# Kernel optimization log

Measured on AMD Instinct MI355X. Metric: run time of the kernel, lower is better.

## Reference

```python
import jax, jax.numpy as jnp
import numpy as np

N0, N1, N2 = 20000, 15000, 15000
N = N0 + N1 + N2          # total nodes
E = 800000                # edges
H, D = 4, 64              # heads, hidden per head
ED = 64                   # edge feature dim
NET = 8                   # num edge types
C = 16                    # num classes
SLOPE = 0.2               # leaky relu negative slope
ALPHA = 0.05              # residual-attention mixing

def _glorot(key, shape):
    return jax.random.normal(key, shape, dtype=jnp.float32) / jnp.sqrt(jnp.float32(shape[-1]))

def setup_inputs() -> dict:
    key = jax.random.key(0)
    ks = jax.random.split(key, 32)
    return {
        "x0": jax.random.normal(ks[0], (N0, 128), jnp.float32),
        "x1": jax.random.normal(ks[1], (N1, 64), jnp.float32),
        "x2": jax.random.normal(ks[2], (N2, 32), jnp.float32),
        "src": jax.random.randint(ks[3], (E,), 0, N),
        "dst": jax.random.randint(ks[4], (E,), 0, N),
        "efeat": jax.random.randint(ks[5], (E,), 0, NET),
        # per-node-type input projections (fc_list)
        "W0": _glorot(ks[6], (64, 128)), "b0": jnp.zeros((64,), jnp.float32),
        "W1": _glorot(ks[7], (64, 64)),  "b1": jnp.zeros((64,), jnp.float32),
        "W2": _glorot(ks[8], (64, 32)),  "b2": jnp.zeros((64,), jnp.float32),
        # GAT layer 0: in 64 -> H*D, no residual, elu
        "Wg0": _glorot(ks[9], (H * D, 64)),
        "etab0": _glorot(ks[10], (NET, ED)),
        "We0": _glorot(ks[11], (H * ED, ED)),
        "al0": _glorot(ks[12], (H, D)), "ar0": _glorot(ks[13], (H, D)), "ae0": _glorot(ks[14], (H, ED)),
        # GAT layer 1: in H*D -> H*D, identity residual, elu
        "Wg1": _glorot(ks[15], (H * D, H * D)),
        "etab1": _glorot(ks[16], (NET, ED)),
        "We1": _glorot(ks[17], (H * ED, ED)),
        "al1": _glorot(ks[18], (H, D)), "ar1": _glorot(ks[19], (H, D)), "ae1": _glorot(ks[20], (H, ED)),
        # final GAT layer: in H*D -> 1*C, linear residual, no activation
        "Wg2": _glorot(ks[21], (C, H * D)),
        "etab2": _glorot(ks[22], (NET, ED)),
        "We2": _glorot(ks[23], (ED, ED)),
        "al2": _glorot(ks[24], (1, C)), "ar2": _glorot(ks[25], (1, C)), "ae2": _glorot(ks[26], (1, ED)),
        "resW2": _glorot(ks[27], (C, H * D)),
    }

def _edge_softmax(scores, dst):
    # softmax over incoming edges of each dst node; scores: [E, H]
    m = jax.ops.segment_max(scores, dst, num_segments=N)
    ex = jnp.exp(scores - m[dst])
    s = jax.ops.segment_sum(ex, dst, num_segments=N)
    return ex / (s[dst] + 1e-9)

def _gat_conv(h, src, dst, et, Wg, etab, We, al, ar, ae, res_attn, res, resW, act):
    nH, oD = al.shape
    feat = (h @ Wg.T).reshape(N, nH, oD)                 # [N,H,D]
    ee = (etab[et] @ We.T).reshape(E, nH, -1)            # [E,H,ED]
    el = jnp.einsum('nhd,hd->nh', feat, al)
    er = jnp.einsum('nhd,hd->nh', feat, ar)
    es = jnp.einsum('ehd,hd->eh', ee, ae)
    logits = jax.nn.leaky_relu(el[src] + er[dst] + es, SLOPE)
    a = _edge_softmax(logits, dst)                       # [E,H]
    if res_attn is not None:
        a = a * (1.0 - ALPHA) + res_attn * ALPHA
    out = jax.ops.segment_sum(a[:, :, None] * feat[src], dst, num_segments=N)
    if res:
        resval = (h @ resW.T).reshape(N, -1, oD) if resW is not None else h.reshape(N, nH, oD)
        out = out + resval
    if act is not None:
        out = act(out)
    return out, jax.lax.stop_gradient(a)                 # attention detached (res_attn)

def reference(x0, x1, x2, src, dst, efeat, W0, b0, W1, b1, W2, b2,
              Wg0, etab0, We0, al0, ar0, ae0,
              Wg1, etab1, We1, al1, ar1, ae1,
              Wg2, etab2, We2, al2, ar2, ae2, resW2):
    h = jnp.concatenate([x0 @ W0.T + b0, x1 @ W1.T + b1, x2 @ W2.T + b2], axis=0)  # [N,64]
    h, ra = _gat_conv(h, src, dst, efeat, Wg0, etab0, We0, al0, ar0, ae0, None, False, None, jax.nn.elu)
    h = h.reshape(N, -1)
    h, ra = _gat_conv(h, src, dst, efeat, Wg1, etab1, We1, al1, ar1, ae1, ra, True, None, jax.nn.elu)
    h = h.reshape(N, -1)
    logits, _ = _gat_conv(h, src, dst, efeat, Wg2, etab2, We2, al2, ar2, ae2, None, True, resW2, None)
    return logits.mean(axis=1)                           # [N, C]
```

## Files before the change

kernel.cpp:

```cpp
#include <hip/hip_runtime.h>
#include <math.h>

#define N0 20000
#define N1 15000
#define N2 15000
#define NN 50000
#define EE 800000
#define SLOPE 0.2f
#define ALPHA 0.05f

typedef _Float16 h8 __attribute__((ext_vector_type(8)));
typedef _Float16 h4 __attribute__((ext_vector_type(4)));
typedef float f4v __attribute__((ext_vector_type(4)));

__device__ __forceinline__ float sel4(float4 v, int h) {
    float lo = (h & 1) ? v.y : v.x;
    float hi = (h & 1) ? v.w : v.z;
    return (h & 2) ? hi : lo;
}

__device__ __forceinline__ float elu_fast(float x) {
    return x > 0.f ? x : __expf(x) - 1.f;
}


__global__ void hist_kernel(const int* __restrict__ dst, int* __restrict__ deg, int E_) {
    int e = blockIdx.x * blockDim.x + threadIdx.x;
    if (e < E_) atomicAdd(&deg[dst[e]], 1);
}

__global__ __launch_bounds__(256) void block_sum_kernel(const int* __restrict__ deg,
                                                        int* __restrict__ bsum, int n) {
    int i = blockIdx.x * 256 + threadIdx.x;
    int v = (i < n) ? deg[i] : 0;
    #pragma unroll
    for (int off = 32; off > 0; off >>= 1) v += __shfl_down(v, off);
    __shared__ int sh[4];
    if ((threadIdx.x & 63) == 0) sh[threadIdx.x >> 6] = v;
    __syncthreads();
    if (threadIdx.x == 0) bsum[blockIdx.x] = sh[0] + sh[1] + sh[2] + sh[3];
}

__global__ __launch_bounds__(256) void scan_bsum_kernel(int* __restrict__ bsum, int nb) {
    __shared__ int sh[256];
    int tid = threadIdx.x;
    int v = (tid < nb) ? bsum[tid] : 0;
    sh[tid] = v;
    __syncthreads();
    #pragma unroll
    for (int off = 1; off < 256; off <<= 1) {
        int t = (tid >= off) ? sh[tid - off] : 0;
        __syncthreads();
        sh[tid] += t;
        __syncthreads();
    }
    if (tid < nb) bsum[tid] = sh[tid] - v;
}

__global__ __launch_bounds__(256) void scan_out_kernel(const int* __restrict__ deg,
                                                       const int* __restrict__ boff,
                                                       int* __restrict__ rowstart,
                                                       int* __restrict__ cursor, int n) {
    __shared__ int sh[256];
    int tid = threadIdx.x;
    int i = blockIdx.x * 256 + tid;
    int v = (i < n) ? deg[i] : 0;
    sh[tid] = v;
    __syncthreads();
    #pragma unroll
    for (int off = 1; off < 256; off <<= 1) {
        int t = (tid >= off) ? sh[tid - off] : 0;
        __syncthreads();
        sh[tid] += t;
        __syncthreads();
    }
    int excl = sh[tid] - v + boff[blockIdx.x];
    if (i < n) { rowstart[i] = excl; cursor[i] = excl; }
    if (i == n - 1) rowstart[n] = excl + v;
}

__global__ void scatter_kernel(const int* __restrict__ src, const int* __restrict__ dst,
                               const int* __restrict__ et, int* __restrict__ cursor,
                               int* __restrict__ pk, int E_) {
    int e = blockIdx.x * blockDim.x + threadIdx.x;
    if (e >= E_) return;
    int d = dst[e];
    int p = atomicAdd(&cursor[d], 1);
    pk[p] = (et[e] << 16) | src[e];
}


__global__ void es_table_all(const float* __restrict__ etab0, const float* __restrict__ We0,
                             const float* __restrict__ ae0,
                             const float* __restrict__ etab1, const float* __restrict__ We1,
                             const float* __restrict__ ae1,
                             const float* __restrict__ etab2, const float* __restrict__ We2,
                             const float* __restrict__ ae2,
                             float* __restrict__ es) {
    int b = blockIdx.x;
    const float *etab, *We, *ae;
    float* out;
    int H;
    if (b < 32)      { etab = etab0; We = We0; ae = ae0; out = es;      H = 4; }
    else if (b < 64) { b -= 32; etab = etab1; We = We1; ae = ae1; out = es + 32; H = 4; }
    else             { b -= 64; etab = etab2; We = We2; ae = ae2; out = es + 64; H = 1; }
    int t = b / H, h = b % H;
    int j = threadIdx.x;
    const float* w = We + (size_t)(h * 64 + j) * 64;
    const float* e = etab + t * 64;
    float s = 0.f;
    #pragma unroll
    for (int k = 0; k < 64; k += 4) {
        float4 wv = *(const float4*)(w + k);
        float4 ev = *(const float4*)(e + k);
        s += wv.x * ev.x + wv.y * ev.y + wv.z * ev.z + wv.w * ev.w;
    }
    s *= ae[h * 64 + j];
    #pragma unroll
    for (int off = 32; off > 0; off >>= 1) s += __shfl_down(s, off);
    if (j == 0) out[t * H + h] = s;
}


__global__ void f2h10(const float* s0, _Float16* d0, int n0,
                      const float* s1, _Float16* d1, int n1,
                      const float* s2, _Float16* d2, int n2,
                      const float* s3, _Float16* d3, int n3,
                      const float* s4, _Float16* d4, int n4,
                      const float* s5, _Float16* d5, int n5,
                      const float* s6, _Float16* d6, int n6,
                      const float* s7, _Float16* d7, int n7,
                      const float* s8, _Float16* d8, int n8,
                      const float* s9, _Float16* d9, int n9) {
    int t = blockIdx.x * 256 + threadIdx.x;
    if (t < n0) { d0[t] = (_Float16)s0[t]; return; } t -= n0;
    if (t < n1) { d1[t] = (_Float16)s1[t]; return; } t -= n1;
    if (t < n2) { d2[t] = (_Float16)s2[t]; return; } t -= n2;
    if (t < n3) { d3[t] = (_Float16)s3[t]; return; } t -= n3;
    if (t < n4) { d4[t] = (_Float16)s4[t]; return; } t -= n4;
    if (t < n5) { d5[t] = (_Float16)s5[t]; return; } t -= n5;
    if (t < n6) { d6[t] = (_Float16)s6[t]; return; } t -= n6;
    if (t < n7) { d7[t] = (_Float16)s7[t]; return; } t -= n7;
    if (t < n8) { d8[t] = (_Float16)s8[t]; return; } t -= n8;
    if (t < n9) { d9[t] = (_Float16)s9[t]; }
}


template<int NT, int ELR>
__device__ __forceinline__ void gemm_body(int bx, int by,
                                          const _Float16* __restrict__ A,
                                          const _Float16* __restrict__ B,
                                          const float* __restrict__ bias,
                                          float* __restrict__ Cf,
                                          _Float16* __restrict__ Ch,
                                          float* __restrict__ el,
                                          float* __restrict__ er,
                                          const float* __restrict__ al,
                                          const float* __restrict__ ar,
                                          int M, int N, int K) {
    const int wave = threadIdx.x >> 6;
    const int lane = threadIdx.x & 63;
    const int m_base = (bx * 4 + wave) * 32;
    const int n_base = by * (NT * 16);
    const int row = lane & 15;
    const int kq = (lane >> 4) * 8;

    f4v acc[2][NT];
    #pragma unroll
    for (int i = 0; i < 2; i++)
        #pragma unroll
        for (int j = 0; j < NT; j++) {
            f4v z = {0.f, 0.f, 0.f, 0.f};
            acc[i][j] = z;
        }

    int ra = m_base + row;      if (ra >= M) ra = M - 1;
    int rb2 = m_base + 16 + row; if (rb2 >= M) rb2 = M - 1;
    const _Float16* a0p = A + (size_t)ra * K + kq;
    const _Float16* a1p = A + (size_t)rb2 * K + kq;
    const _Float16* bp  = B + (size_t)(n_base + row) * K + kq;

    for (int k = 0; k < K; k += 32) {
        h8 a0 = *(const h8*)(a0p + k);
        h8 a1 = *(const h8*)(a1p + k);
        #pragma unroll
        for (int j = 0; j < NT; j++) {
            h8 b = *(const h8*)(bp + (size_t)j * 16 * K + k);
            acc[0][j] = __builtin_amdgcn_mfma_f32_16x16x32_f16(a0, b, acc[0][j], 0, 0, 0);
            acc[1][j] = __builtin_amdgcn_mfma_f32_16x16x32_f16(a1, b, acc[1][j], 0, 0, 0);
        }
    }

    const int col = lane & 15;
    const int rb = (lane >> 4) * 4;

    if (ELR == 1) {
        float alw[NT], arw[NT];
        #pragma unroll
        for (int j = 0; j < NT; j++) {
            int cg = n_base + j * 16 + col;
            int hg = cg >> 6, d = cg & 63;
            alw[j] = al[hg * 64 + d];
            arw[j] = ar[hg * 64 + d];
        }
        const int hb = n_base >> 6;
        #pragma unroll
        for (int ms = 0; ms < 2; ms++) {
            #pragma unroll
            for (int r = 0; r < 4; r++) {
                float e0 = 0.f, e1 = 0.f, f0 = 0.f, f1 = 0.f;
                #pragma unroll
                for (int j = 0; j < NT; j++) {
                    float av = acc[ms][j][r];
                    if (j < NT / 2) { e0 = fmaf(av, alw[j], e0); f0 = fmaf(av, arw[j], f0); }
                    else            { e1 = fmaf(av, alw[j], e1); f1 = fmaf(av, arw[j], f1); }
                }
                #pragma unroll
                for (int off = 1; off <= 8; off <<= 1) {
                    e0 += __shfl_xor(e0, off);
                    e1 += __shfl_xor(e1, off);
                    f0 += __shfl_xor(f0, off);
                    f1 += __shfl_xor(f1, off);
                }
                int m = m_base + ms * 16 + rb + r;
                if (col == 0 && m < M) {
                    el[m * 4 + hb]     = e0;
                    el[m * 4 + hb + 1] = e1;
                    er[m * 4 + hb]     = f0;
                    er[m * 4 + hb + 1] = f1;
                }
            }
        }
    }
    if (ELR == 2) {
        float alw = al[col], arw = ar[col];
        #pragma unroll
        for (int ms = 0; ms < 2; ms++) {
            #pragma unroll
            for (int r = 0; r < 4; r++) {
                float e = acc[ms][0][r] * alw;
                float f = acc[ms][0][r] * arw;
                #pragma unroll
                for (int off = 1; off <= 8; off <<= 1) {
                    e += __shfl_xor(e, off);
                    f += __shfl_xor(f, off);
                }
                int m = m_base + ms * 16 + rb + r;
                if (col == 0 && m < M) { el[m] = e; er[m] = f; }
            }
        }
    }

    #pragma unroll
    for (int ms = 0; ms < 2; ms++) {
        #pragma unroll
        for (int j = 0; j < NT; j++) {
            #pragma unroll
            for (int r = 0; r < 4; r++) {
                int m = m_base + ms * 16 + rb + r;
                if (m < M) {
                    int n = n_base + j * 16 + col;
                    float v = acc[ms][j][r];
                    if (bias) v += bias[n];
                    if (Cf) Cf[(size_t)m * N + n] = v;
                    if (Ch) Ch[(size_t)m * N + n] = (_Float16)v;
                }
            }
        }
    }
}

template<int NT, int ELR>
__global__ __launch_bounds__(256) void gemm_mfma(const _Float16* __restrict__ A,
                                                 const _Float16* __restrict__ B,
                                                 const float* __restrict__ bias,
                                                 float* __restrict__ Cf,
                                                 _Float16* __restrict__ Ch,
                                                 float* __restrict__ el,
                                                 float* __restrict__ er,
                                                 const float* __restrict__ al,
                                                 const float* __restrict__ ar,
                                                 int M, int N, int K) {
    gemm_body<NT, ELR>(blockIdx.x, blockIdx.y, A, B, bias, Cf, Ch, el, er, al, ar, M, N, K);
}

__global__ __launch_bounds__(256) void proj3(const _Float16* __restrict__ x0h, const _Float16* __restrict__ W0h, const float* __restrict__ b0,
                                             const _Float16* __restrict__ x1h, const _Float16* __restrict__ W1h, const float* __restrict__ b1,
                                             const _Float16* __restrict__ x2h, const _Float16* __restrict__ W2h, const float* __restrict__ b2,
                                             _Float16* __restrict__ h0h, int nb0, int nb1) {
    int b = blockIdx.x;
    if (b < nb0) {
        gemm_body<4, 0>(b, 0, x0h, W0h, b0, nullptr, h0h,
                        nullptr, nullptr, nullptr, nullptr, N0, 64, 128);
    } else if (b < nb0 + nb1) {
        gemm_body<4, 0>(b - nb0, 0, x1h, W1h, b1, nullptr, h0h + (size_t)N0 * 64,
                        nullptr, nullptr, nullptr, nullptr, N1, 64, 64);
    } else {
        gemm_body<4, 0>(b - nb0 - nb1, 0, x2h, W2h, b2, nullptr, h0h + (size_t)(N0 + N1) * 64,
                        nullptr, nullptr, nullptr, nullptr, N2, 64, 32);
    }
}


template<bool WRITE_A, bool HAS_PREV, bool HAS_RES>
__global__ __launch_bounds__(256) void gat_fused4(const int* __restrict__ rowstart,
                                                  const int* __restrict__ pk,
                                                  const float* __restrict__ el,
                                                  const float* __restrict__ er,
                                                  const float* __restrict__ es,
                                                  const _Float16* __restrict__ feat,
                                                  const _Float16* __restrict__ aprev,
                                                  _Float16* __restrict__ awrite,
                                                  const _Float16* __restrict__ resh,
                                                  _Float16* __restrict__ outh, int nN) {
    __shared__ int2 as_lds[4][4][66];
    const int wave = threadIdx.x >> 6;
    const int lane = threadIdx.x & 63;
    int n = blockIdx.x * 4 + wave;
    if (n >= nN) return;
    const int r0 = rowstart[n], r1 = rowstart[n + 1];
    const int deg = r1 - r0;
    float4 er4 = *(const float4*)(er + n * 4);

    if (deg <= 64) {
        const int idx = r0 + lane;
        const bool act = idx < r1;
        int p = act ? pk[idx] : 0;
        int psrc = p & 0xFFFF;
        float4 v4 = {-INFINITY, -INFINITY, -INFINITY, -INFINITY};
        if (act) {
            float4 e4 = *(const float4*)(el + psrc * 4);
            float4 c4 = *(const float4*)(es + (p >> 16) * 4);
            float v;
            v = e4.x + er4.x + c4.x; v4.x = v > 0.f ? v : SLOPE * v;
            v = e4.y + er4.y + c4.y; v4.y = v > 0.f ? v : SLOPE * v;
            v = e4.z + er4.z + c4.z; v4.z = v > 0.f ? v : SLOPE * v;
            v = e4.w + er4.w + c4.w; v4.w = v > 0.f ? v : SLOPE * v;
        }
        float4 m4 = v4;
        #pragma unroll
        for (int off = 1; off <= 8; off <<= 1) {
            m4.x = fmaxf(m4.x, __shfl_xor(m4.x, off));
            m4.y = fmaxf(m4.y, __shfl_xor(m4.y, off));
            m4.z = fmaxf(m4.z, __shfl_xor(m4.z, off));
            m4.w = fmaxf(m4.w, __shfl_xor(m4.w, off));
        }
        if (deg > 16) {
            m4.x = fmaxf(m4.x, __shfl_xor(m4.x, 16));
            m4.y = fmaxf(m4.y, __shfl_xor(m4.y, 16));
            m4.z = fmaxf(m4.z, __shfl_xor(m4.z, 16));
            m4.w = fmaxf(m4.w, __shfl_xor(m4.w, 16));
        }
        if (deg > 32) {
            m4.x = fmaxf(m4.x, __shfl_xor(m4.x, 32));
            m4.y = fmaxf(m4.y, __shfl_xor(m4.y, 32));
            m4.z = fmaxf(m4.z, __shfl_xor(m4.z, 32));
            m4.w = fmaxf(m4.w, __shfl_xor(m4.w, 32));
        }
        float4 ex = {0.f, 0.f, 0.f, 0.f};
        if (act) {
            ex.x = __expf(v4.x - m4.x);
            ex.y = __expf(v4.y - m4.y);
            ex.z = __expf(v4.z - m4.z);
            ex.w = __expf(v4.w - m4.w);
        }
        float4 s4 = ex;
        #pragma unroll
        for (int off = 1; off <= 8; off <<= 1) {
            s4.x += __shfl_xor(s4.x, off);
            s4.y += __shfl_xor(s4.y, off);
            s4.z += __shfl_xor(s4.z, off);
            s4.w += __shfl_xor(s4.w, off);
        }
        if (deg > 16) {
            s4.x += __shfl_xor(s4.x, 16);
            s4.y += __shfl_xor(s4.y, 16);
            s4.z += __shfl_xor(s4.z, 16);
            s4.w += __shfl_xor(s4.w, 16);
        }
        if (deg > 32) {
            s4.x += __shfl_xor(s4.x, 32);
            s4.y += __shfl_xor(s4.y, 32);
            s4.z += __shfl_xor(s4.z, 32);
            s4.w += __shfl_xor(s4.w, 32);
        }
        float4 a4;
        a4.x = ex.x / (s4.x + 1e-9f);
        a4.y = ex.y / (s4.y + 1e-9f);
        a4.z = ex.z / (s4.z + 1e-9f);
        a4.w = ex.w / (s4.w + 1e-9f);
        if (HAS_PREV && act) {
            h4 pv = *(const h4*)(aprev + (size_t)idx * 4);
            a4.x = a4.x * (1.f - ALPHA) + ALPHA * (float)pv[0];
            a4.y = a4.y * (1.f - ALPHA) + ALPHA * (float)pv[1];
            a4.z = a4.z * (1.f - ALPHA) + ALPHA * (float)pv[2];
            a4.w = a4.w * (1.f - ALPHA) + ALPHA * (float)pv[3];
        }
        if (WRITE_A && act) {
            h4 aw;
            aw[0] = (_Float16)a4.x; aw[1] = (_Float16)a4.y;
            aw[2] = (_Float16)a4.z; aw[3] = (_Float16)a4.w;
            *(h4*)(awrite + (size_t)idx * 4) = aw;
        }
        as_lds[wave][0][lane] = make_int2(__float_as_int(a4.x), psrc);
        as_lds[wave][1][lane] = make_int2(__float_as_int(a4.y), psrc);
        as_lds[wave][2][lane] = make_int2(__float_as_int(a4.z), psrc);
        as_lds[wave][3][lane] = make_int2(__float_as_int(a4.w), psrc);

        const int half = lane >> 5;
        const int fl = lane & 31;
        const int h = fl >> 3;
        float acc8[8];
        #pragma unroll
        for (int q = 0; q < 8; q++) acc8[q] = 0.f;
        int i = r0;
        for (; i + 7 < r1; i += 8) {
            int j0 = (i - r0) + half;
            int2 e0 = as_lds[wave][h][j0 + 0];
            int2 e1 = as_lds[wave][h][j0 + 2];
            int2 e2 = as_lds[wave][h][j0 + 4];
            int2 e3 = as_lds[wave][h][j0 + 6];
            float a0 = __int_as_float(e0.x), a1 = __int_as_float(e1.x);
            float a2 = __int_as_float(e2.x), a3 = __int_as_float(e3.x);
            h8 f0 = *(const h8*)(feat + (size_t)e0.y * 256 + fl * 8);
            h8 f1 = *(const h8*)(feat + (size_t)e1.y * 256 + fl * 8);
            h8 f2 = *(const h8*)(feat + (size_t)e2.y * 256 + fl * 8);
            h8 f3 = *(const h8*)(feat + (size_t)e3.y * 256 + fl * 8);
            #pragma unroll
            for (int q = 0; q < 8; q++) acc8[q] = fmaf(a0, (float)f0[q], acc8[q]);
            #pragma unroll
            for (int q = 0; q < 8; q++) acc8[q] = fmaf(a1, (float)f1[q], acc8[q]);
            #pragma unroll
            for (int q = 0; q < 8; q++) acc8[q] = fmaf(a2, (float)f2[q], acc8[q]);
            #pragma unroll
            for (int q = 0; q < 8; q++) acc8[q] = fmaf(a3, (float)f3[q], acc8[q]);
        }
        for (; i + 3 < r1; i += 4) {
            int j0 = (i - r0) + half;
            int2 e0 = as_lds[wave][h][j0 + 0];
            int2 e1 = as_lds[wave][h][j0 + 2];
            float a0 = __int_as_float(e0.x), a1 = __int_as_float(e1.x);
            h8 f0 = *(const h8*)(feat + (size_t)e0.y * 256 + fl * 8);
            h8 f1 = *(const h8*)(feat + (size_t)e1.y * 256 + fl * 8);
            #pragma unroll
            for (int q = 0; q < 8; q++) acc8[q] = fmaf(a0, (float)f0[q], acc8[q]);
            #pragma unroll
            for (int q = 0; q < 8; q++) acc8[q] = fmaf(a1, (float)f1[q], acc8[q]);
        }
        for (; i + 1 < r1; i += 2) {
            int j0 = (i - r0) + half;
            int2 e0 = as_lds[wave][h][j0];
            float a0 = __int_as_float(e0.x);
            h8 f0 = *(const h8*)(feat + (size_t)e0.y * 256 + fl * 8);
            #pragma unroll
            for (int q = 0; q < 8; q++) acc8[q] = fmaf(a0, (float)f0[q], acc8[q]);
        }
        if (i < r1) {
            int j0 = i - r0;
            int2 e0 = as_lds[wave][h][j0];
            float a0 = (half == 0) ? __int_as_float(e0.x) : 0.f;
            h8 f0 = *(const h8*)(feat + (size_t)e0.y * 256 + fl * 8);
            #pragma unroll
            for (int q = 0; q < 8; q++) acc8[q] = fmaf(a0, (float)f0[q], acc8[q]);
        }
        #pragma unroll
        for (int q = 0; q < 8; q++) acc8[q] += __shfl_xor(acc8[q], 32);

        if (half == 0) {
            if (HAS_RES) {
                h8 rv = *(const h8*)(resh + (size_t)n * 256 + fl * 8);
                #pragma unroll
                for (int q = 0; q < 8; q++) acc8[q] += (float)rv[q];
            }
            #pragma unroll
            for (int q = 0; q < 8; q++) acc8[q] = elu_fast(acc8[q]);
            h8 o;
            #pragma unroll
            for (int q = 0; q < 8; q++) o[q] = (_Float16)acc8[q];
            *(h8*)(outh + (size_t)n * 256 + fl * 8) = o;
        }
        return;
    }

    float4 m4 = {-INFINITY, -INFINITY, -INFINITY, -INFINITY};
    for (int base = r0; base < r1; base += 64) {
        int idx = base + lane;
        if (idx < r1) {
            int p = pk[idx];
            float4 e4 = *(const float4*)(el + (p & 0xFFFF) * 4);
            float4 c4 = *(const float4*)(es + (p >> 16) * 4);
            float v;
            v = e4.x + er4.x + c4.x; v = v > 0.f ? v : SLOPE * v; m4.x = fmaxf(m4.x, v);
            v = e4.y + er4.y + c4.y; v = v > 0.f ? v : SLOPE * v; m4.y = fmaxf(m4.y, v);
            v = e4.z + er4.z + c4.z; v = v > 0.f ? v : SLOPE * v; m4.z = fmaxf(m4.z, v);
            v = e4.w + er4.w + c4.w; v = v > 0.f ? v : SLOPE * v; m4.w = fmaxf(m4.w, v);
        }
    }
    #pragma unroll
    for (int off = 1; off < 64; off <<= 1) {
        m4.x = fmaxf(m4.x, __shfl_xor(m4.x, off));
        m4.y = fmaxf(m4.y, __shfl_xor(m4.y, off));
        m4.z = fmaxf(m4.z, __shfl_xor(m4.z, off));
        m4.w = fmaxf(m4.w, __shfl_xor(m4.w, off));
    }
    float4 s4 = {0.f, 0.f, 0.f, 0.f};
    for (int base = r0; base < r1; base += 64) {
        int idx = base + lane;
        if (idx < r1) {
            int p = pk[idx];
            float4 e4 = *(const float4*)(el + (p & 0xFFFF) * 4);
            float4 c4 = *(const float4*)(es + (p >> 16) * 4);
            float4 exv;
            float v;
            v = e4.x + er4.x + c4.x; v = v > 0.f ? v : SLOPE * v; exv.x = __expf(v - m4.x);
            v = e4.y + er4.y + c4.y; v = v > 0.f ? v : SLOPE * v; exv.y = __expf(v - m4.y);
            v = e4.z + er4.z + c4.z; v = v > 0.f ? v : SLOPE * v; exv.z = __expf(v - m4.z);
            v = e4.w + er4.w + c4.w; v = v > 0.f ? v : SLOPE * v; exv.w = __expf(v - m4.w);
            if (base == r0) {
                as_lds[wave][0][lane] = make_int2(__float_as_int(exv.x), p & 0xFFFF);
                as_lds[wave][1][lane] = make_int2(__float_as_int(exv.y), p & 0xFFFF);
                as_lds[wave][2][lane] = make_int2(__float_as_int(exv.z), p & 0xFFFF);
                as_lds[wave][3][lane] = make_int2(__float_as_int(exv.w), p & 0xFFFF);
            }
            s4.x += exv.x; s4.y += exv.y; s4.z += exv.z; s4.w += exv.w;
        }
    }
    #pragma unroll
    for (int off = 1; off < 64; off <<= 1) {
        s4.x += __shfl_xor(s4.x, off);
        s4.y += __shfl_xor(s4.y, off);
        s4.z += __shfl_xor(s4.z, off);
        s4.w += __shfl_xor(s4.w, off);
    }
    float4 inv4;
    inv4.x = 1.f / (s4.x + 1e-9f); inv4.y = 1.f / (s4.y + 1e-9f);
    inv4.z = 1.f / (s4.z + 1e-9f); inv4.w = 1.f / (s4.w + 1e-9f);
    {
        int idx = r0 + lane;
        float4 a;
        a.x = __int_as_float(as_lds[wave][0][lane].x) * inv4.x;
        a.y = __int_as_float(as_lds[wave][1][lane].x) * inv4.y;
        a.z = __int_as_float(as_lds[wave][2][lane].x) * inv4.z;
        a.w = __int_as_float(as_lds[wave][3][lane].x) * inv4.w;
        if (HAS_PREV) {
            h4 pv = *(const h4*)(aprev + (size_t)idx * 4);
            a.x = a.x * (1.f - ALPHA) + ALPHA * (float)pv[0];
            a.y = a.y * (1.f - ALPHA) + ALPHA * (float)pv[1];
            a.z = a.z * (1.f - ALPHA) + ALPHA * (float)pv[2];
            a.w = a.w * (1.f - ALPHA) + ALPHA * (float)pv[3];
        }
        if (WRITE_A) {
            h4 aw;
            aw[0] = (_Float16)a.x; aw[1] = (_Float16)a.y;
            aw[2] = (_Float16)a.z; aw[3] = (_Float16)a.w;
            *(h4*)(awrite + (size_t)idx * 4) = aw;
        }
        as_lds[wave][0][lane].x = __float_as_int(a.x);
        as_lds[wave][1][lane].x = __float_as_int(a.y);
        as_lds[wave][2][lane].x = __float_as_int(a.z);
        as_lds[wave][3][lane].x = __float_as_int(a.w);
    }
    if (WRITE_A) {
        for (int base = r0 + 64; base < r1; base += 64) {
            int idx = base + lane;
            if (idx < r1) {
                int p = pk[idx];
                float4 e4 = *(const float4*)(el + (p & 0xFFFF) * 4);
                float4 c4 = *(const float4*)(es + (p >> 16) * 4);
                float4 a;
                float v;
                v = e4.x + er4.x + c4.x; v = v > 0.f ? v : SLOPE * v; a.x = __expf(v - m4.x) * inv4.x;
                v = e4.y + er4.y + c4.y; v = v > 0.f ? v : SLOPE * v; a.y = __expf(v - m4.y) * inv4.y;
                v = e4.z + er4.z + c4.z; v = v > 0.f ? v : SLOPE * v; a.z = __expf(v - m4.z) * inv4.z;
                v = e4.w + er4.w + c4.w; v = v > 0.f ? v : SLOPE * v; a.w = __expf(v - m4.w) * inv4.w;
                if (HAS_PREV) {
                    h4 pv = *(const h4*)(aprev + (size_t)idx * 4);
                    a.x = a.x * (1.f - ALPHA) + ALPHA * (float)pv[0];
                    a.y = a.y * (1.f - ALPHA) + ALPHA * (float)pv[1];
                    a.z = a.z * (1.f - ALPHA) + ALPHA * (float)pv[2];
                    a.w = a.w * (1.f - ALPHA) + ALPHA * (float)pv[3];
                }
                h4 aw;
                aw[0] = (_Float16)a.x; aw[1] = (_Float16)a.y;
                aw[2] = (_Float16)a.z; aw[3] = (_Float16)a.w;
                *(h4*)(awrite + (size_t)idx * 4) = aw;
            }
        }
    }
    const int h = lane >> 4;
    float4 acc = {0.f, 0.f, 0.f, 0.f};
    const int cap = r0 + 64;
    for (int i = r0; i < cap; i++) {
        int2 e0 = as_lds[wave][h][i - r0];
        h4 f = *(const h4*)(feat + (size_t)e0.y * 256 + lane * 4);
        float av = __int_as_float(e0.x);
        acc.x = fmaf(av, (float)f[0], acc.x);
        acc.y = fmaf(av, (float)f[1], acc.y);
        acc.z = fmaf(av, (float)f[2], acc.z);
        acc.w = fmaf(av, (float)f[3], acc.w);
    }
    {
        float mh = sel4(m4, h), invh = sel4(inv4, h), erh = sel4(er4, h);
        for (int i = cap; i < r1; i++) {
            int p = pk[i];
            int s = p & 0xFFFF, t = p >> 16;
            float v = el[s * 4 + h] + erh + es[t * 4 + h];
            v = v > 0.f ? v : SLOPE * v;
            float a = __expf(v - mh) * invh;
            if (HAS_PREV) a = a * (1.f - ALPHA) + ALPHA * (float)aprev[(size_t)i * 4 + h];
            h4 f = *(const h4*)(feat + (size_t)s * 256 + lane * 4);
            acc.x = fmaf(a, (float)f[0], acc.x);
            acc.y = fmaf(a, (float)f[1], acc.y);
            acc.z = fmaf(a, (float)f[2], acc.z);
            acc.w = fmaf(a, (float)f[3], acc.w);
        }
    }
    if (HAS_RES) {
        h4 rv = *(const h4*)(resh + (size_t)n * 256 + lane * 4);
        acc.x += (float)rv[0]; acc.y += (float)rv[1];
        acc.z += (float)rv[2]; acc.w += (float)rv[3];
    }
    acc.x = elu_fast(acc.x);
    acc.y = elu_fast(acc.y);
    acc.z = elu_fast(acc.z);
    acc.w = elu_fast(acc.w);
    h4 o;
    o[0] = (_Float16)acc.x; o[1] = (_Float16)acc.y;
    o[2] = (_Float16)acc.z; o[3] = (_Float16)acc.w;
    *(h4*)(outh + (size_t)n * 256 + lane * 4) = o;
}


__global__ __launch_bounds__(256) void gat_fused1(const int* __restrict__ rowstart,
                                                  const int* __restrict__ pk,
                                                  const float* __restrict__ el,
                                                  const float* __restrict__ er,
                                                  const float* __restrict__ es,
                                                  const float* __restrict__ cpack,
                                                  float* __restrict__ out, int nN) {
    const int wave = threadIdx.x >> 6;
    const int lane = threadIdx.x & 63;
    int n = blockIdx.x * 4 + wave;
    if (n >= nN) return;
    const int r0 = rowstart[n], r1 = rowstart[n + 1];
    const int deg = r1 - r0;
    const float ern = er[n];

    if (deg <= 64) {
        const int idx = r0 + lane;
        const bool act = idx < r1;
        int p = act ? pk[idx] : 0;
        int psrc = p & 0xFFFF;
        float v = -INFINITY;
        if (act) {
            float t = el[psrc] + ern + es[p >> 16];
            v = t > 0.f ? t : SLOPE * t;
        }
        float m = v;
        #pragma unroll
        for (int off = 1; off <= 8; off <<= 1) m = fmaxf(m, __shfl_xor(m, off));
        if (deg > 16) m = fmaxf(m, __shfl_xor(m, 16));
        if (deg > 32) m = fmaxf(m, __shfl_xor(m, 32));
        float ex = act ? __expf(v - m) : 0.f;
        float s = ex;
        #pragma unroll
        for (int off = 1; off <= 8; off <<= 1) s += __shfl_xor(s, off);
        if (deg > 16) s += __shfl_xor(s, 16);
        if (deg > 32) s += __shfl_xor(s, 32);
        float a = ex / (s + 1e-9f);

        const int eslot = lane >> 4, fl = lane & 15;
        float acc = 0.f;
        int i = r0;
        for (; i + 7 < r1; i += 8) {
            int j0 = (i - r0) + eslot;
            int j1 = j0 + 4;
            int s0 = __shfl(psrc, j0);
            int s1 = __shfl(psrc, j1);
            float a0 = __shfl(a, j0);
            float a1 = __shfl(a, j1);
            float f0 = cpack[(size_t)s0 * 32 + fl];
            float f1 = cpack[(size_t)s1 * 32 + fl];
            acc = fmaf(a0, f0, acc);
            acc = fmaf(a1, f1, acc);
        }
        for (; i + 3 < r1; i += 4) {
            int j = (i - r0) + eslot;
            int sj = __shfl(psrc, j);
            float aj = __shfl(a, j);
            acc = fmaf(aj, cpack[(size_t)sj * 32 + fl], acc);
        }
        int rem = r1 - i;
        if (rem > 0) {
            int j = (i - r0) + (eslot < rem ? eslot : rem - 1);
            int sj = __shfl(psrc, j);
            float aj = __shfl(a, j);
            if (eslot >= rem) aj = 0.f;
            acc = fmaf(aj, cpack[(size_t)sj * 32 + fl], acc);
        }
        acc += __shfl_xor(acc, 16);
        acc += __shfl_xor(acc, 32);
        if (lane < 16) out[(size_t)n * 16 + lane] = acc + cpack[(size_t)n * 32 + 16 + lane];
        return;
    }

    float m = -INFINITY;
    for (int base = r0; base < r1; base += 64) {
        int idx = base + lane;
        if (idx < r1) {
            int p = pk[idx];
            float v = el[p & 0xFFFF] + ern + es[p >> 16];
            v = v > 0.f ? v : SLOPE * v;
            m = fmaxf(m, v);
        }
    }
    #pragma unroll
    for (int off = 1; off < 64; off <<= 1) m = fmaxf(m, __shfl_xor(m, off));
    float s = 0.f;
    for (int base = r0; base < r1; base += 64) {
        int idx = base + lane;
        if (idx < r1) {
            int p = pk[idx];
            float v = el[p & 0xFFFF] + ern + es[p >> 16];
            v = v > 0.f ? v : SLOPE * v;
            s += __expf(v - m);
        }
    }
    #pragma unroll
    for (int off = 1; off < 64; off <<= 1) s += __shfl_xor(s, off);
    float inv = 1.f / (s + 1e-9f);
    const int eslot = lane >> 4, fl = lane & 15;
    float acc = 0.f;
    for (int i = r0; i < r1; i += 4) {
        int rem = r1 - i;
        if (eslot < rem) {
            int j = i + eslot;
            int p = pk[j];
            float v = el[p & 0xFFFF] + ern + es[p >> 16];
            v = v > 0.f ? v : SLOPE * v;
            float a = __expf(v - m) * inv;
            acc = fmaf(a, cpack[(size_t)(p & 0xFFFF) * 32 + fl], acc);
        }
    }
    acc += __shfl_xor(acc, 16);
    acc += __shfl_xor(acc, 32);
    if (lane < 16) out[(size_t)n * 16 + lane] = acc + cpack[(size_t)n * 32 + 16 + lane];
}


extern "C" void kernel_launch(void* const* d_in, const int* in_sizes, int n_in,
                              void* d_out, int out_size, void* d_ws, size_t ws_size,
                              hipStream_t stream) {
    const float* x0 = (const float*)d_in[0];
    const float* x1 = (const float*)d_in[1];
    const float* x2 = (const float*)d_in[2];
    const int* src  = (const int*)d_in[3];
    const int* dst  = (const int*)d_in[4];
    const int* et   = (const int*)d_in[5];
    const float* W0 = (const float*)d_in[6];  const float* b0 = (const float*)d_in[7];
    const float* W1 = (const float*)d_in[8];  const float* b1 = (const float*)d_in[9];
    const float* W2 = (const float*)d_in[10]; const float* b2 = (const float*)d_in[11];
    const float* Wg0 = (const float*)d_in[12]; const float* etab0 = (const float*)d_in[13];
    const float* We0 = (const float*)d_in[14]; const float* al0 = (const float*)d_in[15];
    const float* ar0 = (const float*)d_in[16]; const float* ae0 = (const float*)d_in[17];
    const float* Wg1 = (const float*)d_in[18]; const float* etab1 = (const float*)d_in[19];
    const float* We1 = (const float*)d_in[20]; const float* al1 = (const float*)d_in[21];
    const float* ar1 = (const float*)d_in[22]; const float* ae1 = (const float*)d_in[23];
    const float* Wg2 = (const float*)d_in[24]; const float* etab2 = (const float*)d_in[25];
    const float* We2 = (const float*)d_in[26]; const float* al2 = (const float*)d_in[27];
    const float* ar2 = (const float*)d_in[28]; const float* ae2 = (const float*)d_in[29];
    const float* resW2 = (const float*)d_in[30];
    float* outp = (float*)d_out;

    char* p = (char*)d_ws;
    auto alloc = [&](size_t bytes) -> void* {
        void* r = (void*)p;
        p += (bytes + 255) & ~(size_t)255;
        return r;
    };
    _Float16* x0h   = (_Float16*)alloc((size_t)N0 * 128 * 2);
    _Float16* x1h   = (_Float16*)alloc((size_t)N1 * 64 * 2);
    _Float16* x2h   = (_Float16*)alloc((size_t)N2 * 32 * 2);
    _Float16* W0h   = (_Float16*)alloc(64 * 128 * 2);
    _Float16* W1h   = (_Float16*)alloc(64 * 64 * 2);
    _Float16* W2h   = (_Float16*)alloc(64 * 32 * 2);
    _Float16* Wg0h  = (_Float16*)alloc(256 * 64 * 2);
    _Float16* Wg1h  = (_Float16*)alloc(256 * 256 * 2);
    _Float16* wpkh  = (_Float16*)alloc(32 * 256 * 2);
    _Float16* h0h   = (_Float16*)alloc((size_t)NN * 64 * 2);
    _Float16* feath = (_Float16*)alloc((size_t)NN * 256 * 2);
    _Float16* bufAh = (_Float16*)alloc((size_t)NN * 256 * 2);
    _Float16* bufBh = (_Float16*)alloc((size_t)NN * 256 * 2);
    _Float16* a0h   = (_Float16*)alloc((size_t)EE * 4 * 2);
    float* el    = (float*)alloc((size_t)NN * 4 * 4);
    float* er    = (float*)alloc((size_t)NN * 4 * 4);
    float* es    = (float*)alloc(96 * 4);
    float* cpack = (float*)alloc((size_t)NN * 32 * 4);
    int* rowstart = (int*)alloc((size_t)(NN + 1) * 4);
    int* deg      = (int*)alloc((size_t)NN * 4);
    int* cursor   = (int*)alloc((size_t)NN * 4);
    int* bsum     = (int*)alloc(256 * 4);
    int* pk       = (int*)alloc((size_t)EE * 4);

    const int EB = (EE + 255) / 256;
    const int NB = (NN + 255) / 256;
    const int MB128 = (NN + 127) / 128;
    const int WB = (NN + 3) / 4;
    const int nb0 = (N0 + 127) / 128;
    const int nb1 = (N1 + 127) / 128;
    const int nb2 = (N2 + 127) / 128;

    hipMemsetAsync(deg, 0, (size_t)NN * 4, stream);
    hist_kernel<<<EB, 256, 0, stream>>>(dst, deg, EE);
    block_sum_kernel<<<NB, 256, 0, stream>>>(deg, bsum, NN);
    scan_bsum_kernel<<<1, 256, 0, stream>>>(bsum, NB);
    scan_out_kernel<<<NB, 256, 0, stream>>>(deg, bsum, rowstart, cursor, NN);
    scatter_kernel<<<EB, 256, 0, stream>>>(src, dst, et, cursor, pk, EE);

    es_table_all<<<72, 64, 0, stream>>>(etab0, We0, ae0, etab1, We1, ae1, etab2, We2, ae2, es);
    {
        int n0c = N0 * 128, n1c = N1 * 64, n2c = N2 * 32;
        int total = n0c + n1c + n2c + 8192 + 4096 + 2048 + 16384 + 65536 + 4096 + 4096;
        f2h10<<<(total + 255) / 256, 256, 0, stream>>>(
            x0, x0h, n0c, x1, x1h, n1c, x2, x2h, n2c,
            W0, W0h, 8192, W1, W1h, 4096, W2, W2h, 2048,
            Wg0, Wg0h, 16384, Wg1, Wg1h, 65536,
            Wg2, wpkh, 4096, resW2, wpkh + 4096, 4096);
    }

    proj3<<<nb0 + nb1 + nb2, 256, 0, stream>>>(x0h, W0h, b0, x1h, W1h, b1, x2h, W2h, b2,
                                               h0h, nb0, nb1);

    gemm_mfma<8, 1><<<dim3(MB128, 2), 256, 0, stream>>>(h0h, Wg0h, nullptr, nullptr, feath,
                                                        el, er, al0, ar0, NN, 256, 64);
    gat_fused4<true, false, false><<<WB, 256, 0, stream>>>(
        rowstart, pk, el, er, es + 0, feath, nullptr, a0h, nullptr, bufAh, NN);

    gemm_mfma<8, 1><<<dim3(MB128, 2), 256, 0, stream>>>(bufAh, Wg1h, nullptr, nullptr, feath,
                                                        el, er, al1, ar1, NN, 256, 256);
    gat_fused4<false, true, true><<<WB, 256, 0, stream>>>(
        rowstart, pk, el, er, es + 32, feath, a0h, nullptr, bufAh, bufBh, NN);

    gemm_mfma<2, 2><<<dim3(MB128, 1), 256, 0, stream>>>(bufBh, wpkh, nullptr, cpack, nullptr,
                                                        el, er, al2, ar2, NN, 32, 256);
    gat_fused1<<<WB, 256, 0, stream>>>(rowstart, pk, el, er, es + 64, cpack, outp, NN);
}
```

Baseline: 480.1 us.

## Merge scan and prep kernels, store final-layer features in fp16

```diff
diff --git a/kernel.cpp b/kernel.cpp
--- a/kernel.cpp
+++ b/kernel.cpp
@@ -41,42 +41,41 @@
     if (threadIdx.x == 0) bsum[blockIdx.x] = sh[0] + sh[1] + sh[2] + sh[3];
 }
 
-__global__ __launch_bounds__(256) void scan_bsum_kernel(int* __restrict__ bsum, int nb) {
-    __shared__ int sh[256];
+__global__ __launch_bounds__(256) void scan_out2(const int* __restrict__ deg,
+                                                 const int* __restrict__ bsum,
+                                                 int* __restrict__ rowstart,
+                                                 int* __restrict__ cursor, int n, int nb) {
+    __shared__ int sb[256];
+    __shared__ int boff_s;
     int tid = threadIdx.x;
     int v = (tid < nb) ? bsum[tid] : 0;
-    sh[tid] = v;
+    sb[tid] = v;
     __syncthreads();
     #pragma unroll
     for (int off = 1; off < 256; off <<= 1) {
-        int t = (tid >= off) ? sh[tid - off] : 0;
+        int t = (tid >= off) ? sb[tid - off] : 0;
         __syncthreads();
-        sh[tid] += t;
+        sb[tid] += t;
         __syncthreads();
     }
-    if (tid < nb) bsum[tid] = sh[tid] - v;
-}
-
-__global__ __launch_bounds__(256) void scan_out_kernel(const int* __restrict__ deg,
-                                                       const int* __restrict__ boff,
-                                                       int* __restrict__ rowstart,
-                                                       int* __restrict__ cursor, int n) {
-    __shared__ int sh[256];
-    int tid = threadIdx.x;
+    if (tid == blockIdx.x) boff_s = sb[tid] - v;
+    __syncthreads();
+    int boff = boff_s;
     int i = blockIdx.x * 256 + tid;
-    int v = (i < n) ? deg[i] : 0;
-    sh[tid] = v;
+    int d = (i < n) ? deg[i] : 0;
     __syncthreads();
+    sb[tid] = d;
+    __syncthreads();
     #pragma unroll
     for (int off = 1; off < 256; off <<= 1) {
-        int t = (tid >= off) ? sh[tid - off] : 0;
+        int t = (tid >= off) ? sb[tid - off] : 0;
         __syncthreads();
-        sh[tid] += t;
+        sb[tid] += t;
         __syncthreads();
     }
-    int excl = sh[tid] - v + boff[blockIdx.x];
+    int excl = sb[tid] - d + boff;
     if (i < n) { rowstart[i] = excl; cursor[i] = excl; }
-    if (i == n - 1) rowstart[n] = excl + v;
+    if (i == n - 1) rowstart[n] = excl + d;
 }
 
 __global__ void scatter_kernel(const int* __restrict__ src, const int* __restrict__ dst,
@@ -90,22 +89,19 @@
 }
 
 
-__global__ void es_table_all(const float* __restrict__ etab0, const float* __restrict__ We0,
-                             const float* __restrict__ ae0,
-                             const float* __restrict__ etab1, const float* __restrict__ We1,
-                             const float* __restrict__ ae1,
-                             const float* __restrict__ etab2, const float* __restrict__ We2,
-                             const float* __restrict__ ae2,
-                             float* __restrict__ es) {
-    int b = blockIdx.x;
+__device__ __forceinline__ void es_pair(int p,
+                                        const float* __restrict__ etab0, const float* __restrict__ We0, const float* __restrict__ ae0,
+                                        const float* __restrict__ etab1, const float* __restrict__ We1, const float* __restrict__ ae1,
+                                        const float* __restrict__ etab2, const float* __restrict__ We2, const float* __restrict__ ae2,
+                                        float* __restrict__ es) {
     const float *etab, *We, *ae;
     float* out;
     int H;
-    if (b < 32)      { etab = etab0; We = We0; ae = ae0; out = es;      H = 4; }
-    else if (b < 64) { b -= 32; etab = etab1; We = We1; ae = ae1; out = es + 32; H = 4; }
-    else             { b -= 64; etab = etab2; We = We2; ae = ae2; out = es + 64; H = 1; }
-    int t = b / H, h = b % H;
-    int j = threadIdx.x;
+    if (p < 32)      { etab = etab0; We = We0; ae = ae0; out = es;      H = 4; }
+    else if (p < 64) { p -= 32; etab = etab1; We = We1; ae = ae1; out = es + 32; H = 4; }
+    else             { p -= 64; etab = etab2; We = We2; ae = ae2; out = es + 64; H = 1; }
+    int t = p / H, h = p % H;
+    int j = threadIdx.x & 63;
     const float* w = We + (size_t)(h * 64 + j) * 64;
     const float* e = etab + t * 64;
     float s = 0.f;
@@ -121,18 +117,28 @@
     if (j == 0) out[t * H + h] = s;
 }
 
-
-__global__ void f2h10(const float* s0, _Float16* d0, int n0,
-                      const float* s1, _Float16* d1, int n1,
-                      const float* s2, _Float16* d2, int n2,
-                      const float* s3, _Float16* d3, int n3,
-                      const float* s4, _Float16* d4, int n4,
-                      const float* s5, _Float16* d5, int n5,
-                      const float* s6, _Float16* d6, int n6,
-                      const float* s7, _Float16* d7, int n7,
-                      const float* s8, _Float16* d8, int n8,
-                      const float* s9, _Float16* d9, int n9) {
-    int t = blockIdx.x * 256 + threadIdx.x;
+__global__ __launch_bounds__(256) void prep_kernel(
+        const float* etab0, const float* We0, const float* ae0,
+        const float* etab1, const float* We1, const float* ae1,
+        const float* etab2, const float* We2, const float* ae2,
+        float* es,
+        const float* s0, _Float16* d0, int n0,
+        const float* s1, _Float16* d1, int n1,
+        const float* s2, _Float16* d2, int n2,
+        const float* s3, _Float16* d3, int n3,
+        const float* s4, _Float16* d4, int n4,
+        const float* s5, _Float16* d5, int n5,
+        const float* s6, _Float16* d6, int n6,
+        const float* s7, _Float16* d7, int n7,
+        const float* s8, _Float16* d8, int n8,
+        const float* s9, _Float16* d9, int n9) {
+    int b = blockIdx.x;
+    if (b < 18) {
+        int p = b * 4 + (threadIdx.x >> 6);
+        if (p < 72) es_pair(p, etab0, We0, ae0, etab1, We1, ae1, etab2, We2, ae2, es);
+        return;
+    }
+    int t = (b - 18) * 256 + threadIdx.x;
     if (t < n0) { d0[t] = (_Float16)s0[t]; return; } t -= n0;
     if (t < n1) { d1[t] = (_Float16)s1[t]; return; } t -= n1;
     if (t < n2) { d2[t] = (_Float16)s2[t]; return; } t -= n2;
@@ -174,7 +180,7 @@
             acc[i][j] = z;
         }
 
-    int ra = m_base + row;      if (ra >= M) ra = M - 1;
+    int ra = m_base + row;       if (ra >= M) ra = M - 1;
     int rb2 = m_base + 16 + row; if (rb2 >= M) rb2 = M - 1;
     const _Float16* a0p = A + (size_t)ra * K + kq;
     const _Float16* a1p = A + (size_t)rb2 * K + kq;
@@ -636,7 +642,7 @@
                                                   const float* __restrict__ el,
                                                   const float* __restrict__ er,
                                                   const float* __restrict__ es,
-                                                  const float* __restrict__ cpack,
+                                                  const _Float16* __restrict__ cpack,
                                                   float* __restrict__ out, int nN) {
     const int wave = threadIdx.x >> 6;
     const int lane = threadIdx.x & 63;
@@ -679,8 +685,8 @@
             int s1 = __shfl(psrc, j1);
             float a0 = __shfl(a, j0);
             float a1 = __shfl(a, j1);
-            float f0 = cpack[(size_t)s0 * 32 + fl];
-            float f1 = cpack[(size_t)s1 * 32 + fl];
+            float f0 = (float)cpack[(size_t)s0 * 32 + fl];
+            float f1 = (float)cpack[(size_t)s1 * 32 + fl];
             acc = fmaf(a0, f0, acc);
             acc = fmaf(a1, f1, acc);
         }
@@ -688,7 +694,7 @@
             int j = (i - r0) + eslot;
             int sj = __shfl(psrc, j);
             float aj = __shfl(a, j);
-            acc = fmaf(aj, cpack[(size_t)sj * 32 + fl], acc);
+            acc = fmaf(aj, (float)cpack[(size_t)sj * 32 + fl], acc);
         }
         int rem = r1 - i;
         if (rem > 0) {
@@ -696,11 +702,11 @@
             int sj = __shfl(psrc, j);
             float aj = __shfl(a, j);
             if (eslot >= rem) aj = 0.f;
-            acc = fmaf(aj, cpack[(size_t)sj * 32 + fl], acc);
+            acc = fmaf(aj, (float)cpack[(size_t)sj * 32 + fl], acc);
         }
         acc += __shfl_xor(acc, 16);
         acc += __shfl_xor(acc, 32);
-        if (lane < 16) out[(size_t)n * 16 + lane] = acc + cpack[(size_t)n * 32 + 16 + lane];
+        if (lane < 16) out[(size_t)n * 16 + lane] = acc + (float)cpack[(size_t)n * 32 + 16 + lane];
         return;
     }
 
@@ -739,12 +745,12 @@
             float v = el[p & 0xFFFF] + ern + es[p >> 16];
             v = v > 0.f ? v : SLOPE * v;
             float a = __expf(v - m) * inv;
-            acc = fmaf(a, cpack[(size_t)(p & 0xFFFF) * 32 + fl], acc);
+            acc = fmaf(a, (float)cpack[(size_t)(p & 0xFFFF) * 32 + fl], acc);
         }
     }
     acc += __shfl_xor(acc, 16);
     acc += __shfl_xor(acc, 32);
-    if (lane < 16) out[(size_t)n * 16 + lane] = acc + cpack[(size_t)n * 32 + 16 + lane];
+    if (lane < 16) out[(size_t)n * 16 + lane] = acc + (float)cpack[(size_t)n * 32 + 16 + lane];
 }
 
 
@@ -792,10 +798,10 @@
     _Float16* bufAh = (_Float16*)alloc((size_t)NN * 256 * 2);
     _Float16* bufBh = (_Float16*)alloc((size_t)NN * 256 * 2);
     _Float16* a0h   = (_Float16*)alloc((size_t)EE * 4 * 2);
+    _Float16* cpackh = (_Float16*)alloc((size_t)NN * 32 * 2);
     float* el    = (float*)alloc((size_t)NN * 4 * 4);
     float* er    = (float*)alloc((size_t)NN * 4 * 4);
     float* es    = (float*)alloc(96 * 4);
-    float* cpack = (float*)alloc((size_t)NN * 32 * 4);
     int* rowstart = (int*)alloc((size_t)(NN + 1) * 4);
     int* deg      = (int*)alloc((size_t)NN * 4);
     int* cursor   = (int*)alloc((size_t)NN * 4);
@@ -813,15 +819,14 @@
     hipMemsetAsync(deg, 0, (size_t)NN * 4, stream);
     hist_kernel<<<EB, 256, 0, stream>>>(dst, deg, EE);
     block_sum_kernel<<<NB, 256, 0, stream>>>(deg, bsum, NN);
-    scan_bsum_kernel<<<1, 256, 0, stream>>>(bsum, NB);
-    scan_out_kernel<<<NB, 256, 0, stream>>>(deg, bsum, rowstart, cursor, NN);
+    scan_out2<<<NB, 256, 0, stream>>>(deg, bsum, rowstart, cursor, NN, NB);
     scatter_kernel<<<EB, 256, 0, stream>>>(src, dst, et, cursor, pk, EE);
 
-    es_table_all<<<72, 64, 0, stream>>>(etab0, We0, ae0, etab1, We1, ae1, etab2, We2, ae2, es);
     {
         int n0c = N0 * 128, n1c = N1 * 64, n2c = N2 * 32;
         int total = n0c + n1c + n2c + 8192 + 4096 + 2048 + 16384 + 65536 + 4096 + 4096;
-        f2h10<<<(total + 255) / 256, 256, 0, stream>>>(
+        prep_kernel<<<18 + (total + 255) / 256, 256, 0, stream>>>(
+            etab0, We0, ae0, etab1, We1, ae1, etab2, We2, ae2, es,
             x0, x0h, n0c, x1, x1h, n1c, x2, x2h, n2c,
             W0, W0h, 8192, W1, W1h, 4096, W2, W2h, 2048,
             Wg0, Wg0h, 16384, Wg1, Wg1h, 65536,
@@ -841,7 +846,7 @@
     gat_fused4<false, true, true><<<WB, 256, 0, stream>>>(
         rowstart, pk, el, er, es + 32, feath, a0h, nullptr, bufAh, bufBh, NN);
 
-    gemm_mfma<2, 2><<<dim3(MB128, 1), 256, 0, stream>>>(bufBh, wpkh, nullptr, cpack, nullptr,
+    gemm_mfma<2, 2><<<dim3(MB128, 1), 256, 0, stream>>>(bufBh, wpkh, nullptr, nullptr, cpackh,
                                                         el, er, al2, ar2, NN, 32, 256);
-    gat_fused1<<<WB, 256, 0, stream>>>(rowstart, pk, el, er, es + 64, cpack, outp, NN);
-}
+    gat_fused1<<<WB, 256, 0, stream>>>(rowstart, pk, el, er, es + 64, cpackh, outp, NN);
+}
```

After: 474.2 us. No clear change (-1.2%).
